# Performance work log

Measured on AMD Instinct MI355X. Metric: run time of the kernel, lower is better.

The kernel has to match this reference:

```python
import jax, jax.numpy as jnp
import numpy as np

B, N, C = 4, 2048, 1024
H = 16
HD = C // H  # 64
THETA = 10000.0


def setup_inputs() -> dict:
    key = jax.random.key(0)
    k1, k2, k3, k4 = jax.random.split(key, 4)
    x = jax.random.normal(k1, (B, N, C), dtype=jnp.float32)
    # Linear-style init scaling to keep activations sane
    w_qkv = jax.random.normal(k2, (3 * C, C), dtype=jnp.float32) * (1.0 / np.sqrt(C))
    w_proj = jax.random.normal(k3, (C, C), dtype=jnp.float32) * (1.0 / np.sqrt(C))
    b_proj = jax.random.normal(k4, (C,), dtype=jnp.float32) * 0.01
    # RoPE frequencies: freqs_cis[n, j] = exp(i * n * theta^(-2j/hd))
    inv_freq = 1.0 / (THETA ** (jnp.arange(0, HD, 2, dtype=jnp.float32) / HD))  # (HD/2,)
    angles = jnp.arange(N, dtype=jnp.float32)[:, None] * inv_freq[None, :]  # (N, HD/2)
    freqs_cos = jnp.cos(angles)
    freqs_sin = jnp.sin(angles)
    return {"x": x, "w_qkv": w_qkv, "w_proj": w_proj, "b_proj": b_proj,
            "freqs_cos": freqs_cos, "freqs_sin": freqs_sin}


def _apply_rope(t, cos, sin):
    # t: (B, N, H, HD) -> complex pairs on last dim
    tr = t.reshape(t.shape[:-1] + (HD // 2, 2))
    a, b = tr[..., 0], tr[..., 1]
    c = cos[None, :, None, :]  # (1, N, 1, HD/2)
    s = sin[None, :, None, :]
    out = jnp.stack([a * c - b * s, a * s + b * c], axis=-1)
    return out.reshape(t.shape)


def reference(x, w_qkv, w_proj, b_proj, freqs_cos, freqs_sin):
    Bx, Nx, Cx = x.shape
    scale = HD ** -0.5
    qkv = jnp.einsum('bnc,dc->bnd', x, w_qkv)  # (B, N, 3C)
    qkv = qkv.reshape(Bx, Nx, 3, H, HD)
    q, k, v = qkv[:, :, 0], qkv[:, :, 1], qkv[:, :, 2]  # (B, N, H, HD)
    q = _apply_rope(q, freqs_cos, freqs_sin)
    k = _apply_rope(k, freqs_cos, freqs_sin)
    # (B, H, N, HD)
    q = q.transpose(0, 2, 1, 3)
    k = k.transpose(0, 2, 1, 3)
    v = v.transpose(0, 2, 1, 3)
    attn = jnp.einsum('bhnd,bhmd->bhnm', q, k) * scale
    attn = jax.nn.softmax(attn, axis=-1)
    out = jnp.einsum('bhnm,bhmd->bhnd', attn, v)  # (B, H, N, HD)
    out = out.transpose(0, 2, 1, 3).reshape(Bx, Nx, Cx)
    return jnp.einsum('bnc,dc->bnd', out, w_proj) + b_proj
```

## Files before the change

### kernel.cpp

```cpp
#include <hip/hip_runtime.h>
#include <hip/hip_bf16.h>
#include <stdint.h>

#define B_  4
#define N_  2048
#define C_  1024
#define H_  16
#define HD_ 64
#define M_  (B_*N_)
#define K3_ (3*C_)

typedef __bf16 bf16;
typedef __bf16 bf16x8 __attribute__((ext_vector_type(8)));
typedef __bf16 bf16x4 __attribute__((ext_vector_type(4)));
typedef float f32x4 __attribute__((ext_vector_type(4)));
typedef float f32x16 __attribute__((ext_vector_type(16)));

#if __has_builtin(__builtin_amdgcn_exp2f)
#define EXP2(x) __builtin_amdgcn_exp2f(x)
#else
#define EXP2(x) exp2f(x)
#endif

__global__ void castk3(const float* __restrict__ a, bf16* __restrict__ oa, int na4,
                       const float* __restrict__ b, bf16* __restrict__ ob, int nb4,
                       const float* __restrict__ c, bf16* __restrict__ oc, int nc4) {
    int total = na4 + nb4 + nc4;
    int stride = gridDim.x * blockDim.x;
    for (int i = blockIdx.x * blockDim.x + threadIdx.x; i < total; i += stride) {
        const float* src; bf16* dst; int j = i;
        if (j < na4)              { src = a; dst = oa; }
        else if ((j -= na4) < nb4){ src = b; dst = ob; }
        else                      { j -= nb4; src = c; dst = oc; }
        float4 v = reinterpret_cast<const float4*>(src)[j];
        bf16x4 o;
        o[0] = (bf16)v.x; o[1] = (bf16)v.y; o[2] = (bf16)v.z; o[3] = (bf16)v.w;
        *reinterpret_cast<bf16x4*>(dst + (size_t)j * 4) = o;
    }
}

__device__ __forceinline__ void gll16(const bf16* g, const bf16* l) {
    __builtin_amdgcn_global_load_lds(
        (const __attribute__((address_space(1))) void*)g,
        (__attribute__((address_space(3))) void*)l, 16, 0, 0);
}

__device__ __forceinline__ uint32_t pkbf(float a, float b) {
    union { bf16 h[2]; uint32_t u; } U;
    U.h[0] = (bf16)a; U.h[1] = (bf16)b;
    return U.u;
}

__device__ __forceinline__ uint32_t pkraw(bf16 a, bf16 b) {
    union { bf16 h[2]; uint32_t u; } U;
    U.h[0] = a; U.h[1] = b;
    return U.u;
}

template<int MODE>
__global__ __launch_bounds__(256, 4)
void gemm_bt(const bf16* __restrict__ A, const bf16* __restrict__ Bm,
             int Nn, int Kk,
             bf16* __restrict__ qout, bf16* __restrict__ kout, bf16* __restrict__ vout,
             const float* __restrict__ fcos, const float* __restrict__ fsin,
             const float* __restrict__ bias, float* __restrict__ Cout)
{
    __shared__ bf16 a_lds[2][128 * 32];
    __shared__ bf16 b_lds[2][128 * 32];
    const int tid  = threadIdx.x;
    const int lane = tid & 63;
    const int w    = tid >> 6;
    const int wr   = w >> 1, wc = w & 1;
    const int ntile = Nn >> 7;
    const int nwg = gridDim.x, cpx = nwg >> 3;
    const int swz = (blockIdx.x & 7) * cpx + (blockIdx.x >> 3);
    const int bx = swz % ntile, by = swz / ntile;
    const int m0 = by * 128, n0 = bx * 128;

    f32x4 acc[4][4] = {};

    const int c0 = tid, c1 = tid + 256;
    const bf16* ga0 = A  + (size_t)(m0 + (c0 >> 2)) * Kk + (c0 & 3) * 8;
    const bf16* ga1 = A  + (size_t)(m0 + (c1 >> 2)) * Kk + (c1 & 3) * 8;
    const bf16* gb0 = Bm + (size_t)(n0 + (c0 >> 2)) * Kk + (c0 & 3) * 8;
    const bf16* gb1 = Bm + (size_t)(n0 + (c1 >> 2)) * Kk + (c1 & 3) * 8;

    const int rA = lane & 15;
    const int kk = (lane >> 4) * 8;

    gll16(ga0, &a_lds[0][w * 512]);
    gll16(ga1, &a_lds[0][w * 512 + 2048]);
    gll16(gb0, &b_lds[0][w * 512]);
    gll16(gb1, &b_lds[0][w * 512 + 2048]);
    __syncthreads();

    for (int k0 = 0; k0 < Kk; k0 += 32) {
        const int cur = (k0 >> 5) & 1, nxt = cur ^ 1;
        if (k0 + 32 < Kk) {
            gll16(ga0 + k0 + 32, &a_lds[nxt][w * 512]);
            gll16(ga1 + k0 + 32, &a_lds[nxt][w * 512 + 2048]);
            gll16(gb0 + k0 + 32, &b_lds[nxt][w * 512]);
            gll16(gb1 + k0 + 32, &b_lds[nxt][w * 512 + 2048]);
        }

        bf16x8 af[4], bfr[4];
#pragma unroll
        for (int m = 0; m < 4; ++m)
            af[m] = *reinterpret_cast<const bf16x8*>(&a_lds[cur][(wr * 64 + m * 16 + rA) * 32 + kk]);
#pragma unroll
        for (int n = 0; n < 4; ++n)
            bfr[n] = *reinterpret_cast<const bf16x8*>(&b_lds[cur][(wc * 64 + n * 16 + rA) * 32 + kk]);
#pragma unroll
        for (int m = 0; m < 4; ++m)
#pragma unroll
            for (int n = 0; n < 4; ++n)
                acc[m][n] = __builtin_amdgcn_mfma_f32_16x16x32_bf16(af[m], bfr[n], acc[m][n], 0, 0, 0);
        __syncthreads();
    }

    if (MODE == 1) {
#pragma unroll
        for (int n = 0; n < 4; ++n) {
            int cg = n0 + wc * 64 + n * 16 + (lane & 15);
            float bv = bias[cg];
#pragma unroll
            for (int m = 0; m < 4; ++m) {
                int rg = m0 + wr * 64 + m * 16 + (lane >> 4) * 4;
#pragma unroll
                for (int r = 0; r < 4; ++r)
                    Cout[(size_t)(rg + r) * Nn + cg] = acc[m][n][r] + bv;
            }
        }
    } else {
        const int part = n0 >> 10;
#pragma unroll
        for (int n = 0; n < 4; ++n) {
            int cg  = n0 + wc * 64 + n * 16 + (lane & 15);
            int rem = cg & 1023;
            int h   = rem >> 6, hd = rem & 63;
#pragma unroll
            for (int m = 0; m < 4; ++m) {
#pragma unroll
                for (int r = 0; r < 4; ++r) {
                    int rg   = m0 + wr * 64 + m * 16 + (lane >> 4) * 4 + r;
                    int b    = rg >> 11, nrow = rg & 2047;
                    float val = acc[m][n][r];
                    size_t oi = ((size_t)(b * 16 + h) * N_ + nrow) * HD_ + hd;
                    if (part == 2) {
                        vout[oi] = (bf16)val;
                    } else {
                        float p   = __shfl_xor(val, 1);
                        float cth = fcos[nrow * 32 + (hd >> 1)];
                        float sth = fsin[nrow * 32 + (hd >> 1)];
                        float o   = (lane & 1) ? (val * cth + p * sth) : (val * cth - p * sth);
                        if (part == 0) { o *= 0.18033688011112042f; qout[oi] = (bf16)o; }
                        else           { kout[oi] = (bf16)o; }
                    }
                }
            }
        }
    }
}

#define NT_ (N_ / 64)
__global__ __launch_bounds__(256, 2)
void attn_kernel(const bf16* __restrict__ Q, const bf16* __restrict__ Kb,
                 const bf16* __restrict__ Vb, bf16* __restrict__ Ob)
{
    __shared__ bf16 k_lds[2][64 * 64];
    __shared__ bf16 vt_lds[2][64 * 64];
    const int tid = threadIdx.x, lane = tid & 63, w = tid >> 6;
    const int h5  = lane >> 5;
    const int l31 = lane & 31;
    const int nqt = N_ / 256;
    const int cpx = gridDim.x >> 3;
    const int swzb = (blockIdx.x & 7) * cpx + (blockIdx.x >> 3);
    const int bh = swzb / nqt, qt = swzb % nqt;
    const size_t base = (size_t)bh * N_ * HD_;
    const int q0 = qt * 256 + w * 64;

    bf16x8 qf[2][4];
#pragma unroll
    for (int h = 0; h < 2; ++h) {
        const bf16* qp = Q + base + (size_t)(q0 + h * 32 + l31) * HD_ + h5 * 8;
#pragma unroll
        for (int t = 0; t < 4; ++t)
            qf[h][t] = *reinterpret_cast<const bf16x8*>(qp + t * 16);
    }

    f32x16 oT[2][2] = {};
    float l0 = 0.f, l1 = 0.f;

    const int kRowA = tid >> 3;
    const int kColA = ((tid & 7) ^ (kRowA & 7)) * 8;
    const int kRowB = kRowA + 32;
    const int kColB = ((tid & 7) ^ (kRowB & 7)) * 8;
    const bf16* kSrcA = Kb + base + (size_t)kRowA * HD_ + kColA;
    const bf16* kSrcB = Kb + base + (size_t)kRowB * HD_ + kColB;

    const int kp = tid & 31, dc = tid >> 5;
    const bf16* vSrc0 = Vb + base + (size_t)(2 * kp) * HD_ + dc * 8;
    const bf16* vSrc1 = vSrc0 + HD_;

#define STORE_VT(bufidx, va, vb) do {                                              \
        char* vtb = reinterpret_cast<char*>(&vt_lds[0][0]) + (bufidx) * 8192;      \
        _Pragma("unroll")                                                          \
        for (int j = 0; j < 8; ++j) {                                              \
            int byteoff = (dc * 8 + j) * 128 + ((4 * kp) ^ (j << 4));              \
            *reinterpret_cast<uint32_t*>(vtb + byteoff) = pkraw((va)[j], (vb)[j]); \
        }                                                                          \
    } while (0)

    bf16x8 v0 = *reinterpret_cast<const bf16x8*>(vSrc0);
    bf16x8 v1 = *reinterpret_cast<const bf16x8*>(vSrc1);
    gll16(kSrcA, &k_lds[0][w * 512]);
    gll16(kSrcB, &k_lds[0][2048 + w * 512]);
    STORE_VT(0, v0, v1);
    __syncthreads();

    for (int it = 0; it < NT_; ++it) {
        const int cur = it & 1, nxt = cur ^ 1;
        const bool more = (it + 1 < NT_);

        if (more) {
            size_t adv = (size_t)(it + 1) * 64 * HD_;
            v0 = *reinterpret_cast<const bf16x8*>(vSrc0 + adv);
            v1 = *reinterpret_cast<const bf16x8*>(vSrc1 + adv);
            gll16(kSrcA + adv, &k_lds[nxt][w * 512]);
            gll16(kSrcB + adv, &k_lds[nxt][2048 + w * 512]);
        }

        const char* kbase  = reinterpret_cast<const char*>(&k_lds[0][0]) + cur * 8192;
        const char* vtbase = reinterpret_cast<const char*>(&vt_lds[0][0]) + cur * 8192;
        float psum0 = 0.f, psum1 = 0.f;

#pragma unroll
        for (int s = 0; s < 2; ++s) {
            f32x16 st0 = {}, st1 = {};
            const int row = s * 32 + l31;
#pragma unroll
            for (int t = 0; t < 4; ++t) {
                int cc = (2 * t + h5) ^ (row & 7);
                bf16x8 kf = *reinterpret_cast<const bf16x8*>(kbase + row * 128 + cc * 16);
                st0 = __builtin_amdgcn_mfma_f32_32x32x16_bf16(kf, qf[0][t], st0, 0, 0, 0);
                st1 = __builtin_amdgcn_mfma_f32_32x32x16_bf16(kf, qf[1][t], st1, 0, 0, 0);
            }

#pragma unroll
            for (int i = 0; i < 16; ++i) st0[i] = EXP2(st0[i]);
#pragma unroll
            for (int i = 0; i < 16; ++i) st1[i] = EXP2(st1[i]);

            float t8[8], u8[8];
#pragma unroll
            for (int i = 0; i < 8; ++i) { t8[i] = st0[i] + st0[i + 8]; u8[i] = st1[i] + st1[i + 8]; }
#pragma unroll
            for (int i = 0; i < 4; ++i) { t8[i] = t8[i] + t8[i + 4];   u8[i] = u8[i] + u8[i + 4]; }
            psum0 += (t8[0] + t8[1]) + (t8[2] + t8[3]);
            psum1 += (u8[0] + u8[1]) + (u8[2] + u8[3]);

            uint32_t pk0[4][2], pk1[4][2];
#pragma unroll
            for (int g = 0; g < 4; ++g) {
                pk0[g][0] = pkbf(st0[4 * g + 0], st0[4 * g + 1]);
                pk0[g][1] = pkbf(st0[4 * g + 2], st0[4 * g + 3]);
                pk1[g][0] = pkbf(st1[4 * g + 0], st1[4 * g + 1]);
                pk1[g][1] = pkbf(st1[4 * g + 2], st1[4 * g + 3]);
            }
#pragma unroll
            for (int tt = 0; tt < 2; ++tt) {
                const int t = 2 * s + tt;
                uint32_t a0 = pk0[2 * tt][0], b0 = pk0[2 * tt + 1][0];
                uint32_t a1 = pk0[2 * tt][1], b1 = pk0[2 * tt + 1][1];
                uint32_t c0 = pk1[2 * tt][0], d0 = pk1[2 * tt + 1][0];
                uint32_t c1 = pk1[2 * tt][1], d1 = pk1[2 * tt + 1][1];
                asm volatile("v_permlane32_swap_b32 %0, %1" : "+v"(a0), "+v"(b0));
                asm volatile("v_permlane32_swap_b32 %0, %1" : "+v"(a1), "+v"(b1));
                asm volatile("v_permlane32_swap_b32 %0, %1" : "+v"(c0), "+v"(d0));
                asm volatile("v_permlane32_swap_b32 %0, %1" : "+v"(c1), "+v"(d1));
                union { uint32_t u[4]; bf16x8 v; } U0, U1;
                U0.u[0] = a0; U0.u[1] = a1; U0.u[2] = b0; U0.u[3] = b1;
                U1.u[0] = c0; U1.u[1] = c1; U1.u[2] = d0; U1.u[3] = d1;
#pragma unroll
                for (int n = 0; n < 2; ++n) {
                    int vrow = n * 32 + l31;
                    int cc   = (2 * t + h5) ^ (vrow & 7);
                    bf16x8 vf = *reinterpret_cast<const bf16x8*>(vtbase + vrow * 128 + cc * 16);
                    oT[0][n] = __builtin_amdgcn_mfma_f32_32x32x16_bf16(vf, U0.v, oT[0][n], 0, 0, 0);
                    oT[1][n] = __builtin_amdgcn_mfma_f32_32x32x16_bf16(vf, U1.v, oT[1][n], 0, 0, 0);
                }
            }

            if (s == 0 && more) STORE_VT(nxt, v0, v1);
        }

        psum0 += __shfl_xor(psum0, 32);
        psum1 += __shfl_xor(psum1, 32);
        l0 += psum0;
        l1 += psum1;

        __syncthreads();
    }

    const int b = bh >> 4, hh = bh & 15;
#pragma unroll
    for (int h = 0; h < 2; ++h) {
        float inv = 1.0f / (h ? l1 : l0);
        int q = q0 + h * 32 + l31;
#pragma unroll
        for (int n = 0; n < 2; ++n)
#pragma unroll
            for (int g = 0; g < 4; ++g) {
                int d = n * 32 + 8 * g + 4 * h5;
                bf16x4 o4;
#pragma unroll
                for (int r = 0; r < 4; ++r) o4[r] = (bf16)(oT[h][n][4 * g + r] * inv);
                *reinterpret_cast<bf16x4*>(Ob + ((size_t)(b * N_ + q)) * C_ + hh * 64 + d) = o4;
            }
    }
#undef STORE_VT
}

extern "C" void kernel_launch(void* const* d_in, const int* in_sizes, int n_in,
                              void* d_out, int out_size, void* d_ws, size_t ws_size,
                              hipStream_t stream) {
    const float* x     = (const float*)d_in[0];
    const float* wqkv  = (const float*)d_in[1];
    const float* wproj = (const float*)d_in[2];
    const float* bproj = (const float*)d_in[3];
    const float* fcos  = (const float*)d_in[4];
    const float* fsin  = (const float*)d_in[5];
    float* out = (float*)d_out;

    bf16* x_bf     = (bf16*)d_ws;
    bf16* wqkv_bf  = x_bf    + (size_t)M_ * C_;
    bf16* wproj_bf = wqkv_bf + (size_t)K3_ * C_;
    bf16* qbuf     = wproj_bf + (size_t)C_ * C_;
    bf16* kbuf     = qbuf  + (size_t)M_ * C_;
    bf16* vbuf     = kbuf  + (size_t)M_ * C_;
    bf16* abuf     = vbuf  + (size_t)M_ * C_;

    castk3<<<2048, 256, 0, stream>>>(x,     x_bf,     M_ * C_ / 4,
                                     wqkv,  wqkv_bf,  K3_ * C_ / 4,
                                     wproj, wproj_bf, C_ * C_ / 4);

    gemm_bt<0><<<64 * 24, 256, 0, stream>>>(x_bf, wqkv_bf, K3_, C_,
                                            qbuf, kbuf, vbuf, fcos, fsin, nullptr, nullptr);
    attn_kernel<<<64 * 8, 256, 0, stream>>>(qbuf, kbuf, vbuf, abuf);
    gemm_bt<1><<<64 * 8, 256, 0, stream>>>(abuf, wproj_bf, C_, C_,
                                           nullptr, nullptr, nullptr, nullptr, nullptr, bproj, out);
}
```

Before: 218.9 us.

## Double GEMM K-tile to 64 with XOR-swizzled LDS layout

The GEMM main loop now stages 64-wide K slices per iteration instead of 32, which halves the number of barriers and loop iterations. The LDS layout uses an XOR swizzle on 16-byte chunks to avoid bank conflicts on the wider rows. LDS use per block doubles to 64KB, and launch bounds drop occupancy from 4 to 2 blocks per CU, so there is less latency hiding from concurrent blocks.

```diff
diff --git a/kernel.cpp b/kernel.cpp
--- a/kernel.cpp
+++ b/kernel.cpp
@@ -58,15 +58,15 @@
 }
 
 template<int MODE>
-__global__ __launch_bounds__(256, 4)
+__global__ __launch_bounds__(256, 2)
 void gemm_bt(const bf16* __restrict__ A, const bf16* __restrict__ Bm,
              int Nn, int Kk,
              bf16* __restrict__ qout, bf16* __restrict__ kout, bf16* __restrict__ vout,
              const float* __restrict__ fcos, const float* __restrict__ fsin,
              const float* __restrict__ bias, float* __restrict__ Cout)
 {
-    __shared__ bf16 a_lds[2][128 * 32];
-    __shared__ bf16 b_lds[2][128 * 32];
+    __shared__ bf16 a_lds[2][128 * 64];
+    __shared__ bf16 b_lds[2][128 * 64];
     const int tid  = threadIdx.x;
     const int lane = tid & 63;
     const int w    = tid >> 6;
@@ -79,44 +79,51 @@
 
     f32x4 acc[4][4] = {};
 
-    const int c0 = tid, c1 = tid + 256;
-    const bf16* ga0 = A  + (size_t)(m0 + (c0 >> 2)) * Kk + (c0 & 3) * 8;
-    const bf16* ga1 = A  + (size_t)(m0 + (c1 >> 2)) * Kk + (c1 & 3) * 8;
-    const bf16* gb0 = Bm + (size_t)(n0 + (c0 >> 2)) * Kk + (c0 & 3) * 8;
-    const bf16* gb1 = Bm + (size_t)(n0 + (c1 >> 2)) * Kk + (c1 & 3) * 8;
-
-    const int rA = lane & 15;
-    const int kk = (lane >> 4) * 8;
-
-    gll16(ga0, &a_lds[0][w * 512]);
-    gll16(ga1, &a_lds[0][w * 512 + 2048]);
-    gll16(gb0, &b_lds[0][w * 512]);
-    gll16(gb1, &b_lds[0][w * 512 + 2048]);
+    const int srow = tid >> 3;
+    const int scol = ((tid & 7) ^ (srow & 7)) * 8;
+    const bf16* gaS = A  + (size_t)(m0 + srow) * Kk + scol;
+    const bf16* gbS = Bm + (size_t)(n0 + srow) * Kk + scol;
+    const size_t rj = (size_t)32 * Kk;
+
+#define STAGE_G(slot, koff) do {                                               \
+        _Pragma("unroll")                                                      \
+        for (int j = 0; j < 4; ++j) {                                          \
+            gll16(gaS + (koff) + j * rj, &a_lds[slot][w * 512 + j * 2048]);    \
+            gll16(gbS + (koff) + j * rj, &b_lds[slot][w * 512 + j * 2048]);    \
+        }                                                                      \
+    } while (0)
+
+    const int rA = lane & 15, hi = lane >> 4;
+    const int x7 = rA & 7;
+
+    STAGE_G(0, 0);
     __syncthreads();
 
-    for (int k0 = 0; k0 < Kk; k0 += 32) {
-        const int cur = (k0 >> 5) & 1, nxt = cur ^ 1;
-        if (k0 + 32 < Kk) {
-            gll16(ga0 + k0 + 32, &a_lds[nxt][w * 512]);
-            gll16(ga1 + k0 + 32, &a_lds[nxt][w * 512 + 2048]);
-            gll16(gb0 + k0 + 32, &b_lds[nxt][w * 512]);
-            gll16(gb1 + k0 + 32, &b_lds[nxt][w * 512 + 2048]);
-        }
-
-        bf16x8 af[4], bfr[4];
-#pragma unroll
-        for (int m = 0; m < 4; ++m)
-            af[m] = *reinterpret_cast<const bf16x8*>(&a_lds[cur][(wr * 64 + m * 16 + rA) * 32 + kk]);
-#pragma unroll
-        for (int n = 0; n < 4; ++n)
-            bfr[n] = *reinterpret_cast<const bf16x8*>(&b_lds[cur][(wc * 64 + n * 16 + rA) * 32 + kk]);
-#pragma unroll
-        for (int m = 0; m < 4; ++m)
+    for (int k0 = 0; k0 < Kk; k0 += 64) {
+        const int cur = (k0 >> 6) & 1, nxt = cur ^ 1;
+        if (k0 + 64 < Kk) STAGE_G(nxt, k0 + 64);
+
+        const char* aB = reinterpret_cast<const char*>(&a_lds[cur][0]);
+        const char* bB = reinterpret_cast<const char*>(&b_lds[cur][0]);
+#pragma unroll
+        for (int ks = 0; ks < 2; ++ks) {
+            const int cc = ((ks * 4 + hi) ^ x7) * 16;
+            bf16x8 af[4], bfr[4];
+#pragma unroll
+            for (int m = 0; m < 4; ++m)
+                af[m] = *reinterpret_cast<const bf16x8*>(aB + (wr * 64 + m * 16 + rA) * 128 + cc);
 #pragma unroll
             for (int n = 0; n < 4; ++n)
-                acc[m][n] = __builtin_amdgcn_mfma_f32_16x16x32_bf16(af[m], bfr[n], acc[m][n], 0, 0, 0);
+                bfr[n] = *reinterpret_cast<const bf16x8*>(bB + (wc * 64 + n * 16 + rA) * 128 + cc);
+#pragma unroll
+            for (int m = 0; m < 4; ++m)
+#pragma unroll
+                for (int n = 0; n < 4; ++n)
+                    acc[m][n] = __builtin_amdgcn_mfma_f32_16x16x32_bf16(af[m], bfr[n], acc[m][n], 0, 0, 0);
+        }
         __syncthreads();
     }
+#undef STAGE_G
 
     if (MODE == 1) {
 #pragma unroll
```

After: 220.6 us. About the same (+0.8%).
